# Optimization experiments

Hardware: AMD Instinct MI355X
Metric: run time of the kernel (lower is better)

Reference implementation:

```python
import jax, jax.numpy as jnp
import numpy as np

EPS = 1e-12  # torch F.normalize eps

def _conv1x1(x, w, b=None):
    # x: [B,C,H,W], w: [O,C] -> [B,O,H,W]
    y = jnp.einsum('bchw,oc->bohw', x, w)
    if b is not None:
        y = y + b[None, :, None, None]
    return y

def _l2norm(t):
    n = jnp.sqrt(jnp.sum(t * t, axis=-1, keepdims=True))
    return t / jnp.maximum(n, EPS)

def _gqa(x, w_qkv, w_proj, b_proj, heads=8):
    B, C, H, W = x.shape
    hd = C // heads
    S = H * W
    scale = hd ** -0.5
    qkv = _conv1x1(x, w_qkv)                       # [B,3C,H,W]
    qkv = qkv.reshape(B, 3, heads, hd, S)
    qkv = jnp.transpose(qkv, (0, 1, 2, 4, 3))      # [B,3,h,S,hd]
    q, k, v = qkv[:, 0], qkv[:, 1], qkv[:, 2]
    q = _l2norm(q)
    k = _l2norm(k)
    # group loop in original is just a partition of heads -> batch all heads
    attn = jnp.einsum('bhqd,bhkd->bhqk', q, k) * scale
    attn = jax.nn.softmax(attn, axis=-1)
    out = jnp.einsum('bhqk,bhkd->bhqd', attn, v)   # [B,h,S,hd]
    out = jnp.transpose(out, (0, 1, 3, 2)).reshape(B, C, H, W)
    return _conv1x1(out, w_proj, b_proj)

def _avg_pool(x, s):
    B, C, H, W = x.shape
    return x.reshape(B, C, H // s, s, W // s, s).mean(axis=(3, 5))

def _forward(x, w_qkv_l, w_proj_l, b_proj_l, w_qkv_g, w_proj_g, b_proj_g,
             w_f1, b_f1, w_f2, b_f2, stride=4, heads=8):
    local = _gqa(x, w_qkv_l, w_proj_l, b_proj_l, heads)
    xc = _avg_pool(x, stride)
    g = _gqa(xc, w_qkv_g, w_proj_g, b_proj_g, heads)
    B, C, H, W = x.shape
    g = jax.image.resize(g, (B, C, H, W), method='bilinear')  # half-pixel = align_corners=False
    h = _conv1x1(jnp.concatenate([local, g], axis=1), w_f1, b_f1)
    h = jax.nn.gelu(h, approximate=False)
    return _conv1x1(h, w_f2, b_f2)

def setup_inputs() -> dict:
    key = jax.random.key(0)
    ks = jax.random.split(key, 11)
    C = 256
    d = {
        'x': jax.random.normal(ks[0], (4, C, 48, 48), jnp.float32),
        'w_qkv_l': jax.random.normal(ks[1], (3 * C, C), jnp.float32) * 0.02,
        'w_proj_l': jax.random.normal(ks[2], (C, C), jnp.float32) * 0.02,
        'b_proj_l': jax.random.normal(ks[3], (C,), jnp.float32) * 0.02,
        'w_qkv_g': jax.random.normal(ks[4], (3 * C, C), jnp.float32) * 0.02,
        'w_proj_g': jax.random.normal(ks[5], (C, C), jnp.float32) * 0.02,
        'b_proj_g': jax.random.normal(ks[6], (C,), jnp.float32) * 0.02,
        'w_f1': jax.random.normal(ks[7], (C, 2 * C), jnp.float32) * 0.02,
        'b_f1': jax.random.normal(ks[8], (C,), jnp.float32) * 0.02,
        'w_f2': jax.random.normal(ks[9], (C, C), jnp.float32) * 0.02,
        'b_f2': jax.random.normal(ks[10], (C,), jnp.float32) * 0.02,
    }
    return d

def reference(x, w_qkv_l, w_proj_l, b_proj_l, w_qkv_g, w_proj_g, b_proj_g,
              w_f1, b_f1, w_f2, b_f2):
    return _forward(x, w_qkv_l, w_proj_l, b_proj_l, w_qkv_g, w_proj_g, b_proj_g,
                    w_f1, b_f1, w_f2, b_f2)
```

## Files before the change

kernel.cpp:

```cpp
#include <hip/hip_runtime.h>
#include <hip/hip_bf16.h>
#include <math.h>

typedef __attribute__((ext_vector_type(8))) short bf16x8;
typedef __attribute__((ext_vector_type(4))) float f32x4;

__device__ inline unsigned short f2bf(float x) {
  __hip_bfloat16 h = __float2bfloat16(x);
  return __builtin_bit_cast(unsigned short, h);
}
__device__ inline float bf2f(unsigned short u) {
  unsigned v = ((unsigned)u) << 16;
  return __builtin_bit_cast(float, v);
}
__device__ inline unsigned cvtpk(float a, float b) {
  unsigned r;
  asm("v_cvt_pk_bf16_f32 %0, %1, %2" : "=v"(r) : "v"(a), "v"(b));
  return r;
}

__global__ __launch_bounds__(256)
void prep_kernel(const float* __restrict__ w0, const float* __restrict__ w1,
                 const float* __restrict__ w2, const float* __restrict__ w3,
                 const float* __restrict__ w4, const float* __restrict__ w5,
                 unsigned short* __restrict__ d0, unsigned short* __restrict__ d1,
                 unsigned short* __restrict__ d2, unsigned short* __restrict__ d3,
                 unsigned short* __restrict__ d4, unsigned short* __restrict__ d5,
                 const float* __restrict__ x, float* __restrict__ xg) {
  int idx = blockIdx.x * 256 + threadIdx.x;
  if (idx < 22528) {
    int r = idx;
    const float* src; unsigned short* dst;
    if (r < 6144) { src = w0; dst = d0; }
    else if (r < 8192) { src = w1; dst = d1; r -= 6144; }
    else if (r < 14336) { src = w2; dst = d2; r -= 8192; }
    else if (r < 16384) { src = w3; dst = d3; r -= 14336; }
    else if (r < 20480) { src = w4; dst = d4; r -= 16384; }
    else { src = w5; dst = d5; r -= 20480; }
    const float* in = src + (size_t)r * 32;
    union { unsigned short u[32]; uint4 q[4]; } H, L;
#pragma unroll
    for (int i = 0; i < 32; ++i) {
      float v = in[i];
      unsigned short h = f2bf(v);
      H.u[i] = h;
      L.u[i] = f2bf(v - bf2f(h));
    }
    uint4* op = (uint4*)(dst + (size_t)r * 64);
#pragma unroll
    for (int q = 0; q < 4; ++q) { op[q] = H.q[q]; op[4 + q] = L.q[q]; }
  } else {
    int p = idx - 22528;
    if (p >= 4 * 256 * 144) return;
    int wc = p % 12;
    int t = p / 12;
    int hc = t % 12;
    int bc = t / 12;
    const float* src = x + ((size_t)bc * 48 + hc * 4) * 48 + wc * 4;
    float s = 0.f;
#pragma unroll
    for (int dy = 0; dy < 4; ++dy)
#pragma unroll
      for (int dx = 0; dx < 4; ++dx) s += src[dy * 48 + dx];
    xg[p] = s * (1.0f / 16.0f);
  }
}

template<int ACT, int OT, int CKS, int UPS, typename XT, typename YT>
__device__ __forceinline__
void conv_body(const unsigned short* __restrict__ Whl, const XT* __restrict__ X,
               const float* __restrict__ lpart, const float* __restrict__ bias,
               YT* __restrict__ Y, const float* __restrict__ gsm,
               int Cin, int S, size_t XbS, size_t YbS,
               int bx, int by, int bz, int tid) {
  constexpr int OI = OT / 64;
  __shared__ __align__(16) unsigned short Bs[64 * 32];
  const int w = tid >> 6, lane = tid & 63;
  const int g = lane >> 4, c = lane & 15;
  const int s0 = bx * 64;
  const int o0 = by * OT;
  const int b = bz;
  const int KB = Cin >> 5;
  const int sRow = tid & 63;
  const int jS = tid >> 6;
  const int ss = s0 + sRow;
  const bool sIn = (ss < S);
  unsigned short* BsRow = Bs + sRow * 32;
  const int hiOff = (jS ^ ((sRow >> 1) & 3)) * 8;

  int t00 = 0, t01 = 0, t10 = 0, t11 = 0;
  float w00 = 0.f, w01 = 0.f, w10 = 0.f, w11 = 0.f;
  if constexpr (UPS) {
    if (sIn) {
      int yo = ss / 48, xo = ss % 48;
      float sy = 0.25f * yo - 0.375f;
      float sx = 0.25f * xo - 0.375f;
      int y0 = (int)floorf(sy); float fy = sy - (float)y0;
      int x0 = (int)floorf(sx); float fx = sx - (float)x0;
      int y0c = min(11, max(0, y0)), y1c = min(11, max(0, y0 + 1));
      int x0c = min(11, max(0, x0)), x1c = min(11, max(0, x0 + 1));
      t00 = y0c * 12 + x0c; t01 = y0c * 12 + x1c;
      t10 = y1c * 12 + x0c; t11 = y1c * 12 + x1c;
      w00 = (1.f - fy) * (1.f - fx); w01 = (1.f - fy) * fx;
      w10 = fy * (1.f - fx);         w11 = fy * fx;
    }
  }

  f32x4 acc[OI][4];
#pragma unroll
  for (int oi = 0; oi < OI; ++oi)
#pragma unroll
    for (int si = 0; si < 4; ++si) acc[oi][si] = (f32x4){0.f, 0.f, 0.f, 0.f};

  for (int kb = 0; kb < KB; ++kb) {
    union { unsigned u[4]; bf16x8 v; } hu;
    if (sIn) {
      if constexpr (CKS > 0) {
        const float* xp = (const float*)X + (size_t)b * XbS +
                          (size_t)(kb * 32 + 8 * jS) * S + ss;
        const float* lp = lpart + ((size_t)b * 8 + kb) * S + ss;
        float den = 0.f;
        float num[8] = {0.f, 0.f, 0.f, 0.f, 0.f, 0.f, 0.f, 0.f};
#pragma unroll
        for (int ksi = 0; ksi < CKS; ++ksi) {
          den += lp[(size_t)ksi * 32 * S];
#pragma unroll
          for (int i = 0; i < 8; ++i)
            num[i] += xp[(size_t)(ksi * 1024 + i) * S];
        }
        float rd = 1.0f / den;
#pragma unroll
        for (int i = 0; i < 4; ++i)
          hu.u[i] = cvtpk(num[2 * i] * rd, num[2 * i + 1] * rd);
      } else if constexpr (UPS) {
        if (kb < 8) {
          const XT* xp = X + (size_t)b * XbS + (size_t)(kb * 32 + 8 * jS) * S + ss;
#pragma unroll
          for (int i = 0; i < 4; ++i) {
            unsigned lo = *(const unsigned short*)(xp + (size_t)(2 * i) * S);
            unsigned hi = *(const unsigned short*)(xp + (size_t)(2 * i + 1) * S);
            hu.u[i] = lo | (hi << 16);
          }
        } else {
          const float* gbb = gsm + (size_t)b * 256 * 144 +
                             (size_t)((kb - 8) * 32 + 8 * jS) * 144;
#pragma unroll
          for (int i = 0; i < 4; ++i) {
            const float* g0 = gbb + (size_t)(2 * i) * 144;
            const float* g1 = gbb + (size_t)(2 * i + 1) * 144;
            float v0 = w00 * g0[t00] + w01 * g0[t01] + w10 * g0[t10] + w11 * g0[t11];
            float v1 = w00 * g1[t00] + w01 * g1[t01] + w10 * g1[t10] + w11 * g1[t11];
            hu.u[i] = cvtpk(v0, v1);
          }
        }
      } else if constexpr (sizeof(XT) == 2) {
        const XT* xp = X + (size_t)b * XbS + (size_t)(kb * 32 + 8 * jS) * S + ss;
#pragma unroll
        for (int i = 0; i < 4; ++i) {
          unsigned lo = *(const unsigned short*)(xp + (size_t)(2 * i) * S);
          unsigned hi = *(const unsigned short*)(xp + (size_t)(2 * i + 1) * S);
          hu.u[i] = lo | (hi << 16);
        }
      } else {
        const float* xp = (const float*)X + (size_t)b * XbS +
                          (size_t)(kb * 32 + 8 * jS) * S + ss;
#pragma unroll
        for (int i = 0; i < 4; ++i)
          hu.u[i] = cvtpk(xp[(size_t)(2 * i) * S], xp[(size_t)(2 * i + 1) * S]);
      }
    } else {
#pragma unroll
      for (int i = 0; i < 4; ++i) hu.u[i] = 0;
    }
    bf16x8 ahi[OI], alo[OI];
#pragma unroll
    for (int oi = 0; oi < OI; ++oi) {
      const unsigned short* ap =
          Whl + ((size_t)(o0 + 16 * OI * w + 16 * oi + c) * KB + kb) * 64;
      ahi[oi] = *(const bf16x8*)(ap + 8 * g);
      alo[oi] = *(const bf16x8*)(ap + 32 + 8 * g);
    }
    __syncthreads();
    *(bf16x8*)(BsRow + hiOff) = hu.v;
    __syncthreads();
    bf16x8 bhi[4];
#pragma unroll
    for (int si = 0; si < 4; ++si) {
      int row = 16 * si + c;
      const unsigned short* bp = Bs + row * 32;
      bhi[si] = *(const bf16x8*)(bp + ((g ^ ((row >> 1) & 3)) * 8));
    }
#pragma unroll
    for (int oi = 0; oi < OI; ++oi)
#pragma unroll
      for (int si = 0; si < 4; ++si) {
        acc[oi][si] = __builtin_amdgcn_mfma_f32_16x16x32_bf16(ahi[oi], bhi[si], acc[oi][si], 0, 0, 0);
        acc[oi][si] = __builtin_amdgcn_mfma_f32_16x16x32_bf16(alo[oi], bhi[si], acc[oi][si], 0, 0, 0);
      }
  }
#pragma unroll
  for (int oi = 0; oi < OI; ++oi) {
#pragma unroll
    for (int r = 0; r < 4; ++r) {
      int o = o0 + 16 * OI * w + 16 * oi + 4 * g + r;
      float bv = bias ? bias[o] : 0.f;
#pragma unroll
      for (int si = 0; si < 4; ++si) {
        int s = s0 + 16 * si + c;
        if (s < S) {
          float v = acc[oi][si][r] + bv;
          if (ACT == 1) v = v * 0.5f * (1.0f + erff(v * 0.70710678118654752f));
          if constexpr (sizeof(YT) == 2)
            Y[(size_t)b * YbS + (size_t)o * S + s] = (YT)f2bf(v);
          else
            Y[(size_t)b * YbS + (size_t)o * S + s] = v;
        }
      }
    }
  }
}

__global__ __launch_bounds__(256)
void qkv_conv_kernel(const unsigned short* __restrict__ Wl, const float* __restrict__ Xl,
                     float* __restrict__ Yl,
                     const unsigned short* __restrict__ Wg, const float* __restrict__ Xg,
                     float* __restrict__ Yg) {
  if (blockIdx.y < 6) {
    conv_body<0, 128, 0, 0, float, float>(Wl, Xl, nullptr, nullptr, Yl, nullptr,
        256, 2304, (size_t)256 * 2304, (size_t)768 * 2304,
        blockIdx.x, blockIdx.y, blockIdx.z, threadIdx.x);
  } else {
    if (blockIdx.x >= 3) return;
    conv_body<0, 128, 0, 0, float, float>(Wg, Xg, nullptr, nullptr, Yg, nullptr,
        256, 144, (size_t)256 * 144, (size_t)768 * 144,
        blockIdx.x, blockIdx.y - 6, blockIdx.z, threadIdx.x);
  }
}

__global__ __launch_bounds__(256)
void proj_conv_kernel(const unsigned short* __restrict__ Wl, const float* __restrict__ opl,
                      const float* __restrict__ lpl, const float* __restrict__ bl,
                      unsigned short* __restrict__ cat,
                      const unsigned short* __restrict__ Wg, const float* __restrict__ opg,
                      const float* __restrict__ lpg, const float* __restrict__ bg,
                      float* __restrict__ gsm) {
  if (blockIdx.y < 4) {
    conv_body<0, 64, 3, 0, float, unsigned short>(Wl, opl, lpl, bl, cat, nullptr,
        256, 2304, (size_t)256 * 2304, (size_t)256 * 2304,
        blockIdx.x, blockIdx.y, blockIdx.z, threadIdx.x);
  } else {
    if (blockIdx.x >= 3) return;
    conv_body<0, 64, 3, 0, float, float>(Wg, opg, lpg, bg, gsm, nullptr,
        256, 144, (size_t)256 * 144, (size_t)256 * 144,
        blockIdx.x, blockIdx.y - 4, blockIdx.z, threadIdx.x);
  }
}

__global__ __launch_bounds__(256)
void f1_conv_kernel(const unsigned short* __restrict__ W, const unsigned short* __restrict__ cat,
                    const float* __restrict__ gsm, const float* __restrict__ bias,
                    unsigned short* __restrict__ hbuf) {
  conv_body<1, 64, 0, 1, unsigned short, unsigned short>(W, cat, nullptr, bias, hbuf, gsm,
      512, 2304, (size_t)256 * 2304, (size_t)256 * 2304,
      blockIdx.x, blockIdx.y, blockIdx.z, threadIdx.x);
}

__global__ __launch_bounds__(256)
void f2_conv_kernel(const unsigned short* __restrict__ W, const unsigned short* __restrict__ hbuf,
                    const float* __restrict__ bias, float* __restrict__ out) {
  conv_body<0, 64, 0, 0, unsigned short, float>(W, hbuf, nullptr, bias, out, nullptr,
      256, 2304, (size_t)256 * 2304, (size_t)256 * 2304,
      blockIdx.x, blockIdx.y, blockIdx.z, threadIdx.x);
}

__device__ __forceinline__
void l2n_body(const float* __restrict__ qkv, unsigned short* __restrict__ qd,
              unsigned short* __restrict__ kd, int S, int Sp, int idx) {
  int s = idx % Sp; int t = idx / Sp;
  int h = t & 7; t >>= 3;
  int qk = t & 1; int b = t >> 1;
  if (b >= 4) return;
  unsigned short* dst;
  int srow;
  if (qk == 0) { dst = qd; srow = s; }
  else {
    dst = kd;
    int blk = s >> 6, j = s & 63;
    srow = (blk << 6) + 32 * ((j >> 2) & 1) + 16 * (j >> 5) + 4 * ((j >> 3) & 3) + (j & 3);
  }
  unsigned wbuf[16];
  if (s < S) {
    const float* base = qkv + ((size_t)b * 768 + qk * 256 + h * 32) * S + s;
    float v[32]; float ss = 0.f;
#pragma unroll
    for (int d = 0; d < 32; ++d) { v[d] = base[(size_t)d * S]; ss += v[d] * v[d]; }
    float inv = 1.0f / fmaxf(sqrtf(ss), 1e-12f);
    if (qk == 0) inv *= 0.25506607138105343f;
#pragma unroll
    for (int i = 0; i < 16; ++i) wbuf[i] = cvtpk(v[2 * i] * inv, v[2 * i + 1] * inv);
  } else {
#pragma unroll
    for (int i = 0; i < 16; ++i) wbuf[i] = 0u;
  }
  uint4* o = (uint4*)(dst + ((size_t)(b * 8 + h) * Sp + srow) * 32);
#pragma unroll
  for (int i = 0; i < 4; ++i)
    o[i] = make_uint4(wbuf[4 * i], wbuf[4 * i + 1], wbuf[4 * i + 2], wbuf[4 * i + 3]);
}

__device__ __forceinline__
void vcvt_body(const float* __restrict__ qkv, unsigned short* __restrict__ vt,
               int S, int Sp, int idx) {
  int SpH = Sp >> 1;
  int sp = idx % SpH; int t = idx / SpH;
  int d = t & 31; t >>= 5;
  int h = t & 7; int b = t >> 3;
  if (b >= 4) return;
  const float* src = qkv + ((size_t)b * 768 + 512 + h * 32 + d) * S;
  int s2 = 2 * sp;
  float a = (s2 < S) ? src[s2] : 0.f;
  float c = (s2 + 1 < S) ? src[s2 + 1] : 0.f;
  *(unsigned*)(vt + ((size_t)(b * 8 + h) * 32 + d) * Sp + s2) = cvtpk(a, c);
}

__global__ __launch_bounds__(256)
void cvt_kernel(const float* __restrict__ qkv_l, unsigned short* __restrict__ qr_l,
                unsigned short* __restrict__ kr_l, unsigned short* __restrict__ vt_l,
                const float* __restrict__ qkv_g, unsigned short* __restrict__ qr_g,
                unsigned short* __restrict__ kr_g, unsigned short* __restrict__ vt_g) {
  const int L1 = 2 * 8 * 4 * 2304;
  const int L2 = 4 * 8 * 32 * 1152;
  const int L3 = 2 * 8 * 4 * 256;
  const int L4 = 4 * 8 * 32 * 128;
  int idx = blockIdx.x * 256 + threadIdx.x;
  if (idx < L1) l2n_body(qkv_l, qr_l, kr_l, 2304, 2304, idx);
  else if (idx < L1 + L2) vcvt_body(qkv_l, vt_l, 2304, 2304, idx - L1);
  else if (idx < L1 + L2 + L3) l2n_body(qkv_g, qr_g, kr_g, 144, 256, idx - L1 - L2);
  else if (idx < L1 + L2 + L3 + L4) vcvt_body(qkv_g, vt_g, 144, 256, idx - L1 - L2 - L3);
}

template<int KS>
__device__ __forceinline__
void attn_body(const unsigned short* __restrict__ qr, const unsigned short* __restrict__ kr,
               const unsigned short* __restrict__ vt, float* __restrict__ opart,
               float* __restrict__ lpart, int S, int Sp, int qblk, int ks,
               int h, int b, int tidx) {
  int w = tidx >> 6, lane = tidx & 63;
  int g = lane >> 4, c = lane & 15;
  int q0 = qblk * 256 + w * 64;
  const int chunks = Sp >> 6;
  const int c0 = (ks * chunks) / KS, c1 = ((ks + 1) * chunks) / KS;
  const unsigned short* qbh = qr + (size_t)(b * 8 + h) * Sp * 32;
  const unsigned short* kbh = kr + (size_t)(b * 8 + h) * Sp * 32;
  const unsigned short* vbh = vt + (size_t)(b * 8 + h) * 32 * Sp;

  bf16x8 qf[4];
#pragma unroll
  for (int f = 0; f < 4; ++f)
    qf[f] = *(const bf16x8*)(qbh + (size_t)(q0 + 16 * f + c) * 32 + 8 * g);

  f32x4 oacc[4][2];
#pragma unroll
  for (int f = 0; f < 4; ++f) {
    oacc[f][0] = (f32x4){0.f, 0.f, 0.f, 0.f};
    oacc[f][1] = (f32x4){0.f, 0.f, 0.f, 0.f};
  }
  float ls[4] = {0.f, 0.f, 0.f, 0.f};

  bf16x8 kf[4];
  {
    int k0 = c0 * 64;
#pragma unroll
    for (int t = 0; t < 4; ++t)
      kf[t] = *(const bf16x8*)(kbh + (size_t)(k0 + 16 * t + c) * 32 + 8 * g);
  }

  for (int ch = c0; ch < c1; ++ch) {
    int k0 = ch * 64;
    const f32x4 z = {0.f, 0.f, 0.f, 0.f};
    bool full = (k0 + 64 <= S);
    bf16x8 vf00 = *(const bf16x8*)(vbh + (size_t)c * Sp + k0 + 8 * g);
    bf16x8 vf01 = *(const bf16x8*)(vbh + (size_t)(16 + c) * Sp + k0 + 8 * g);
    bf16x8 vf10 = *(const bf16x8*)(vbh + (size_t)c * Sp + k0 + 32 + 8 * g);
    bf16x8 vf11 = *(const bf16x8*)(vbh + (size_t)(16 + c) * Sp + k0 + 32 + 8 * g);

    f32x4 sL[4], sH[4];
    __builtin_amdgcn_s_setprio(1);
#pragma unroll
    for (int f = 0; f < 4; ++f) {
      sL[f] = __builtin_amdgcn_mfma_f32_16x16x32_bf16(kf[0], qf[f], z, 0, 0, 0);
      sH[f] = __builtin_amdgcn_mfma_f32_16x16x32_bf16(kf[2], qf[f], z, 0, 0, 0);
    }
    __builtin_amdgcn_s_setprio(0);
    union { bf16x8 v; unsigned u[4]; } pf[4];
    if (full) {
#pragma unroll
      for (int f = 0; f < 4; ++f) {
        float e0 = __builtin_amdgcn_exp2f(sL[f][0]);
        float e1 = __builtin_amdgcn_exp2f(sL[f][1]);
        float e2 = __builtin_amdgcn_exp2f(sL[f][2]);
        float e3 = __builtin_amdgcn_exp2f(sL[f][3]);
        float e4 = __builtin_amdgcn_exp2f(sH[f][0]);
        float e5 = __builtin_amdgcn_exp2f(sH[f][1]);
        float e6 = __builtin_amdgcn_exp2f(sH[f][2]);
        float e7 = __builtin_amdgcn_exp2f(sH[f][3]);
        ls[f] += ((e0 + e1) + (e2 + e3)) + ((e4 + e5) + (e6 + e7));
        pf[f].u[0] = cvtpk(e0, e1); pf[f].u[1] = cvtpk(e2, e3);
        pf[f].u[2] = cvtpk(e4, e5); pf[f].u[3] = cvtpk(e6, e7);
      }
    } else {
#pragma unroll
      for (int f = 0; f < 4; ++f) {
        float e[8];
#pragma unroll
        for (int r = 0; r < 4; ++r) {
          int keyL = k0 + 8 * g + r;
          int keyH = k0 + 8 * g + 4 + r;
          e[r]     = (keyL < S) ? __builtin_amdgcn_exp2f(sL[f][r]) : 0.f;
          e[4 + r] = (keyH < S) ? __builtin_amdgcn_exp2f(sH[f][r]) : 0.f;
        }
        ls[f] += ((e[0] + e[1]) + (e[2] + e[3])) + ((e[4] + e[5]) + (e[6] + e[7]));
        pf[f].u[0] = cvtpk(e[0], e[1]); pf[f].u[1] = cvtpk(e[2], e[3]);
        pf[f].u[2] = cvtpk(e[4], e[5]); pf[f].u[3] = cvtpk(e[6], e[7]);
      }
    }
    __builtin_amdgcn_s_setprio(1);
#pragma unroll
    for (int f = 0; f < 4; ++f) {
      oacc[f][0] = __builtin_amdgcn_mfma_f32_16x16x32_bf16(vf00, pf[f].v, oacc[f][0], 0, 0, 0);
      oacc[f][1] = __builtin_amdgcn_mfma_f32_16x16x32_bf16(vf01, pf[f].v, oacc[f][1], 0, 0, 0);
    }
#pragma unroll
    for (int f = 0; f < 4; ++f) {
      sL[f] = __builtin_amdgcn_mfma_f32_16x16x32_bf16(kf[1], qf[f], z, 0, 0, 0);
      sH[f] = __builtin_amdgcn_mfma_f32_16x16x32_bf16(kf[3], qf[f], z, 0, 0, 0);
    }
    __builtin_amdgcn_s_setprio(0);
    if (ch + 1 < c1) {
      int kn = (ch + 1) * 64;
#pragma unroll
      for (int t = 0; t < 4; ++t)
        kf[t] = *(const bf16x8*)(kbh + (size_t)(kn + 16 * t + c) * 32 + 8 * g);
    }
    if (full) {
#pragma unroll
      for (int f = 0; f < 4; ++f) {
        float e0 = __builtin_amdgcn_exp2f(sL[f][0]);
        float e1 = __builtin_amdgcn_exp2f(sL[f][1]);
        float e2 = __builtin_amdgcn_exp2f(sL[f][2]);
        float e3 = __builtin_amdgcn_exp2f(sL[f][3]);
        float e4 = __builtin_amdgcn_exp2f(sH[f][0]);
        float e5 = __builtin_amdgcn_exp2f(sH[f][1]);
        float e6 = __builtin_amdgcn_exp2f(sH[f][2]);
        float e7 = __builtin_amdgcn_exp2f(sH[f][3]);
        ls[f] += ((e0 + e1) + (e2 + e3)) + ((e4 + e5) + (e6 + e7));
        pf[f].u[0] = cvtpk(e0, e1); pf[f].u[1] = cvtpk(e2, e3);
        pf[f].u[2] = cvtpk(e4, e5); pf[f].u[3] = cvtpk(e6, e7);
      }
    } else {
#pragma unroll
      for (int f = 0; f < 4; ++f) {
        float e[8];
#pragma unroll
        for (int r = 0; r < 4; ++r) {
          int keyL = k0 + 32 + 8 * g + r;
          int keyH = k0 + 32 + 8 * g + 4 + r;
          e[r]     = (keyL < S) ? __builtin_amdgcn_exp2f(sL[f][r]) : 0.f;
          e[4 + r] = (keyH < S) ? __builtin_amdgcn_exp2f(sH[f][r]) : 0.f;
        }
        ls[f] += ((e[0] + e[1]) + (e[2] + e[3])) + ((e[4] + e[5]) + (e[6] + e[7]));
        pf[f].u[0] = cvtpk(e[0], e[1]); pf[f].u[1] = cvtpk(e[2], e[3]);
        pf[f].u[2] = cvtpk(e[4], e[5]); pf[f].u[3] = cvtpk(e[6], e[7]);
      }
    }
    __builtin_amdgcn_s_setprio(1);
#pragma unroll
    for (int f = 0; f < 4; ++f) {
      oacc[f][0] = __builtin_amdgcn_mfma_f32_16x16x32_bf16(vf10, pf[f].v, oacc[f][0], 0, 0, 0);
      oacc[f][1] = __builtin_amdgcn_mfma_f32_16x16x32_bf16(vf11, pf[f].v, oacc[f][1], 0, 0, 0);
    }
    __builtin_amdgcn_s_setprio(0);
  }
#pragma unroll
  for (int f = 0; f < 4; ++f) {
    ls[f] += __shfl_xor(ls[f], 16, 64);
    ls[f] += __shfl_xor(ls[f], 32, 64);
  }
  size_t obase = ((size_t)(ks * 4 + b) * 256 + h * 32) * S;
#pragma unroll
  for (int f = 0; f < 4; ++f) {
    int q = q0 + 16 * f + c;
    if (q < S) {
#pragma unroll
      for (int r = 0; r < 4; ++r) {
        opart[obase + (size_t)(4 * g + r) * S + q]      = oacc[f][0][r];
        opart[obase + (size_t)(16 + 4 * g + r) * S + q] = oacc[f][1][r];
      }
    }
  }
  if (lane < 16) {
    size_t lb = ((size_t)(ks * 4 + b) * 8 + h) * S;
#pragma unroll
    for (int f = 0; f < 4; ++f)
      if (q0 + 16 * f + lane < S) lpart[lb + q0 + 16 * f + lane] = ls[f];
  }
}

__global__ __launch_bounds__(256)
void attn_merged_kernel(const unsigned short* __restrict__ qr_l,
                        const unsigned short* __restrict__ kr_l,
                        const unsigned short* __restrict__ vt_l,
                        float* __restrict__ op_l, float* __restrict__ lp_l,
                        const unsigned short* __restrict__ qr_g,
                        const unsigned short* __restrict__ kr_g,
                        const unsigned short* __restrict__ vt_g,
                        float* __restrict__ op_g, float* __restrict__ lp_g) {
  int h = blockIdx.x, b = blockIdx.z, y = blockIdx.y;
  if (y < 27)
    attn_body<3>(qr_l, kr_l, vt_l, op_l, lp_l, 2304, 2304, y / 3, y % 3, h, b, threadIdx.x);
  else
    attn_body<3>(qr_g, kr_g, vt_g, op_g, lp_g, 144, 256, 0, y - 27, h, b, threadIdx.x);
}

extern "C" void kernel_launch(void* const* d_in, const int* in_sizes, int n_in,
                              void* d_out, int out_size, void* d_ws, size_t ws_size,
                              hipStream_t stream) {
  const float* x        = (const float*)d_in[0];
  const float* w_qkv_l  = (const float*)d_in[1];
  const float* w_proj_l = (const float*)d_in[2];
  const float* b_proj_l = (const float*)d_in[3];
  const float* w_qkv_g  = (const float*)d_in[4];
  const float* w_proj_g = (const float*)d_in[5];
  const float* b_proj_g = (const float*)d_in[6];
  const float* w_f1     = (const float*)d_in[7];
  const float* b_f1     = (const float*)d_in[8];
  const float* w_f2     = (const float*)d_in[9];
  const float* b_f2     = (const float*)d_in[10];
  float* out = (float*)d_out;

  const int S = 2304, Sg = 144, B = 4;
  const int Sp = 2304, Sgp = 256;
  const int KS = 3;

  char* wsp = (char*)d_ws;
  size_t off = 0;
  auto alloc = [&](size_t bytes) { char* p = wsp + off; off = (off + bytes + 255) & ~(size_t)255; return p; };
  float* qkv_l = (float*)alloc((size_t)B * 768 * S * 4);
  unsigned short* cat = (unsigned short*)alloc((size_t)B * 256 * S * 2);
  unsigned short* hbuf = (unsigned short*)alloc((size_t)B * 256 * S * 2);
  float* xg    = (float*)alloc((size_t)B * 256 * Sg * 4);
  float* qkv_g = (float*)alloc((size_t)B * 768 * Sg * 4);
  float* gsm   = (float*)alloc((size_t)B * 256 * Sg * 4);
  unsigned short* qr_l = (unsigned short*)alloc((size_t)B * 8 * Sp * 32 * 2);
  unsigned short* kr_l = (unsigned short*)alloc((size_t)B * 8 * Sp * 32 * 2);
  unsigned short* vt_l = (unsigned short*)alloc((size_t)B * 8 * Sp * 32 * 2);
  unsigned short* qr_g = (unsigned short*)alloc((size_t)B * 8 * Sgp * 32 * 2);
  unsigned short* kr_g = (unsigned short*)alloc((size_t)B * 8 * Sgp * 32 * 2);
  unsigned short* vt_g = (unsigned short*)alloc((size_t)B * 8 * Sgp * 32 * 2);
  unsigned short* whl_qkv_l  = (unsigned short*)alloc((size_t)768 * 256 * 2 * 2);
  unsigned short* whl_proj_l = (unsigned short*)alloc((size_t)256 * 256 * 2 * 2);
  unsigned short* whl_qkv_g  = (unsigned short*)alloc((size_t)768 * 256 * 2 * 2);
  unsigned short* whl_proj_g = (unsigned short*)alloc((size_t)256 * 256 * 2 * 2);
  unsigned short* whl_f1     = (unsigned short*)alloc((size_t)256 * 512 * 2 * 2);
  unsigned short* whl_f2     = (unsigned short*)alloc((size_t)256 * 256 * 2 * 2);
  float* lpart_l = (float*)alloc((size_t)KS * B * 8 * S * 4);
  float* lpart_g = (float*)alloc((size_t)KS * B * 8 * Sg * 4);
  float* opart_l = qkv_l;
  float* opart_g = qkv_g;

  dim3 blk(256);

  prep_kernel<<<dim3(664), blk, 0, stream>>>(
      w_qkv_l, w_proj_l, w_qkv_g, w_proj_g, w_f1, w_f2,
      whl_qkv_l, whl_proj_l, whl_qkv_g, whl_proj_g, whl_f1, whl_f2, x, xg);

  qkv_conv_kernel<<<dim3(36, 12, B), blk, 0, stream>>>(
      whl_qkv_l, x, qkv_l, whl_qkv_g, xg, qkv_g);

  cvt_kernel<<<dim3(5760), blk, 0, stream>>>(
      qkv_l, qr_l, kr_l, vt_l, qkv_g, qr_g, kr_g, vt_g);

  attn_merged_kernel<<<dim3(8, 30, B), blk, 0, stream>>>(
      qr_l, kr_l, vt_l, opart_l, lpart_l, qr_g, kr_g, vt_g, opart_g, lpart_g);

  proj_conv_kernel<<<dim3(36, 8, B), blk, 0, stream>>>(
      whl_proj_l, opart_l, lpart_l, b_proj_l, cat,
      whl_proj_g, opart_g, lpart_g, b_proj_g, gsm);

  f1_conv_kernel<<<dim3(36, 4, B), blk, 0, stream>>>(
      whl_f1, cat, gsm, b_f1, hbuf);

  f2_conv_kernel<<<dim3(36, 4, B), blk, 0, stream>>>(
      whl_f2, hbuf, b_f2, out);
}
```

Measured before the change: 142.2 us.

## Fuse L2-normalize and bf16 conversion into QKV conv epilogue, drop cvt kernel

The QKV 1x1 conv now writes normalized, scaled bf16 Q and permuted K rows, plus transposed bf16 V, directly from its accumulators. This removes the separate cvt kernel and the fp32 qkv round trip through global memory. The attention kernel also computes the softmax row sums with an extra MFMA against a ones vector instead of scalar adds and shuffles, and gains a launch-bounds occupancy hint. In exchange, the conv epilogue does more per-block work and scattered 4-byte stores, and opart now needs its own workspace buffer.

Measured after the change: 210.5 us. 1.48x slower.

```diff
diff --git a/kernel.cpp b/kernel.cpp
--- a/kernel.cpp
+++ b/kernel.cpp
@@ -66,11 +66,13 @@
   }
 }
 
-template<int ACT, int OT, int CKS, int UPS, typename XT, typename YT>
+template<int ACT, int OT, int CKS, int UPS, int EPI, typename XT, typename YT>
 __device__ __forceinline__
 void conv_body(const unsigned short* __restrict__ Whl, const XT* __restrict__ X,
                const float* __restrict__ lpart, const float* __restrict__ bias,
                YT* __restrict__ Y, const float* __restrict__ gsm,
+               unsigned short* __restrict__ qd, unsigned short* __restrict__ kd,
+               unsigned short* __restrict__ vt, int Sp,
                int Cin, int S, size_t XbS, size_t YbS,
                int bx, int by, int bz, int tid) {
   constexpr int OI = OT / 64;
@@ -198,6 +200,60 @@
         acc[oi][si] = __builtin_amdgcn_mfma_f32_16x16x32_bf16(alo[oi], bhi[si], acc[oi][si], 0, 0, 0);
       }
   }
+
+  if constexpr (EPI == 1) {
+    int sec = o0 >> 8;
+    int h = ((o0 >> 5) & 7) + w;
+    if (sec == 2) {
+      unsigned short* vb = vt + (size_t)(b * 8 + h) * 32 * Sp;
+#pragma unroll
+      for (int oi = 0; oi < OI; ++oi)
+#pragma unroll
+        for (int r = 0; r < 4; ++r) {
+          int d = 16 * oi + 4 * g + r;
+#pragma unroll
+          for (int si = 0; si < 4; ++si) {
+            int s = s0 + 16 * si + c;
+            if (s < S) vb[(size_t)d * Sp + s] = f2bf(acc[oi][si][r]);
+          }
+        }
+    } else {
+      float invs[4];
+#pragma unroll
+      for (int si = 0; si < 4; ++si) {
+        float t = 0.f;
+#pragma unroll
+        for (int oi = 0; oi < OI; ++oi)
+#pragma unroll
+          for (int r = 0; r < 4; ++r) t += acc[oi][si][r] * acc[oi][si][r];
+        t += __shfl_xor(t, 16, 64);
+        t += __shfl_xor(t, 32, 64);
+        float inv = 1.0f / fmaxf(sqrtf(t), 1e-12f);
+        if (sec == 0) inv *= 0.25506607138105343f;
+        invs[si] = inv;
+      }
+      unsigned short* dstp = (sec == 0) ? qd : kd;
+#pragma unroll
+      for (int si = 0; si < 4; ++si) {
+        int s = s0 + 16 * si + c;
+        if (s >= S) continue;
+        int srow = s;
+        if (sec == 1) {
+          int blk2 = s >> 6, j = s & 63;
+          srow = (blk2 << 6) + 32 * ((j >> 2) & 1) + 16 * (j >> 5) + 4 * ((j >> 3) & 3) + (j & 3);
+        }
+        unsigned short* rowp = dstp + ((size_t)(b * 8 + h) * Sp + srow) * 32;
+#pragma unroll
+        for (int oi = 0; oi < OI; ++oi) {
+          int d0 = 16 * oi + 4 * g;
+          *(unsigned*)(rowp + d0)     = cvtpk(acc[oi][si][0] * invs[si], acc[oi][si][1] * invs[si]);
+          *(unsigned*)(rowp + d0 + 2) = cvtpk(acc[oi][si][2] * invs[si], acc[oi][si][3] * invs[si]);
+        }
+      }
+    }
+    return;
+  }
+
 #pragma unroll
   for (int oi = 0; oi < OI; ++oi) {
 #pragma unroll
@@ -222,17 +278,21 @@
 
 __global__ __launch_bounds__(256)
 void qkv_conv_kernel(const unsigned short* __restrict__ Wl, const float* __restrict__ Xl,
-                     float* __restrict__ Yl,
+                     unsigned short* __restrict__ qr_l, unsigned short* __restrict__ kr_l,
+                     unsigned short* __restrict__ vt_l,
                      const unsigned short* __restrict__ Wg, const float* __restrict__ Xg,
-                     float* __restrict__ Yg) {
+                     unsigned short* __restrict__ qr_g, unsigned short* __restrict__ kr_g,
+                     unsigned short* __restrict__ vt_g) {
   if (blockIdx.y < 6) {
-    conv_body<0, 128, 0, 0, float, float>(Wl, Xl, nullptr, nullptr, Yl, nullptr,
-        256, 2304, (size_t)256 * 2304, (size_t)768 * 2304,
+    conv_body<0, 128, 0, 0, 1, float, float>(Wl, Xl, nullptr, nullptr, (float*)nullptr, nullptr,
+        qr_l, kr_l, vt_l, 2304,
+        256, 2304, (size_t)256 * 2304, 0,
         blockIdx.x, blockIdx.y, blockIdx.z, threadIdx.x);
   } else {
     if (blockIdx.x >= 3) return;
-    conv_body<0, 128, 0, 0, float, float>(Wg, Xg, nullptr, nullptr, Yg, nullptr,
-        256, 144, (size_t)256 * 144, (size_t)768 * 144,
+    conv_body<0, 128, 0, 0, 1, float, float>(Wg, Xg, nullptr, nullptr, (float*)nullptr, nullptr,
+        qr_g, kr_g, vt_g, 256,
+        256, 144, (size_t)256 * 144, 0,
         blockIdx.x, blockIdx.y - 6, blockIdx.z, threadIdx.x);
   }
 }
@@ -245,12 +305,14 @@
                       const float* __restrict__ lpg, const float* __restrict__ bg,
                       float* __restrict__ gsm) {
   if (blockIdx.y < 4) {
-    conv_body<0, 64, 3, 0, float, unsigned short>(Wl, opl, lpl, bl, cat, nullptr,
+    conv_body<0, 64, 3, 0, 0, float, unsigned short>(Wl, opl, lpl, bl, cat, nullptr,
+        nullptr, nullptr, nullptr, 0,
         256, 2304, (size_t)256 * 2304, (size_t)256 * 2304,
         blockIdx.x, blockIdx.y, blockIdx.z, threadIdx.x);
   } else {
     if (blockIdx.x >= 3) return;
-    conv_body<0, 64, 3, 0, float, float>(Wg, opg, lpg, bg, gsm, nullptr,
+    conv_body<0, 64, 3, 0, 0, float, float>(Wg, opg, lpg, bg, gsm, nullptr,
+        nullptr, nullptr, nullptr, 0,
         256, 144, (size_t)256 * 144, (size_t)256 * 144,
         blockIdx.x, blockIdx.y - 4, blockIdx.z, threadIdx.x);
   }
@@ -260,7 +322,8 @@
 void f1_conv_kernel(const unsigned short* __restrict__ W, const unsigned short* __restrict__ cat,
                     const float* __restrict__ gsm, const float* __restrict__ bias,
                     unsigned short* __restrict__ hbuf) {
-  conv_body<1, 64, 0, 1, unsigned short, unsigned short>(W, cat, nullptr, bias, hbuf, gsm,
+  conv_body<1, 64, 0, 1, 0, unsigned short, unsigned short>(W, cat, nullptr, bias, hbuf, gsm,
+      nullptr, nullptr, nullptr, 0,
       512, 2304, (size_t)256 * 2304, (size_t)256 * 2304,
       blockIdx.x, blockIdx.y, blockIdx.z, threadIdx.x);
 }
@@ -268,75 +331,10 @@
 __global__ __launch_bounds__(256)
 void f2_conv_kernel(const unsigned short* __restrict__ W, const unsigned short* __restrict__ hbuf,
                     const float* __restrict__ bias, float* __restrict__ out) {
-  conv_body<0, 64, 0, 0, unsigned short, float>(W, hbuf, nullptr, bias, out, nullptr,
+  conv_body<0, 64, 0, 0, 0, unsigned short, float>(W, hbuf, nullptr, bias, out, nullptr,
+      nullptr, nullptr, nullptr, 0,
       256, 2304, (size_t)256 * 2304, (size_t)256 * 2304,
       blockIdx.x, blockIdx.y, blockIdx.z, threadIdx.x);
-}
-
-__device__ __forceinline__
-void l2n_body(const float* __restrict__ qkv, unsigned short* __restrict__ qd,
-              unsigned short* __restrict__ kd, int S, int Sp, int idx) {
-  int s = idx % Sp; int t = idx / Sp;
-  int h = t & 7; t >>= 3;
-  int qk = t & 1; int b = t >> 1;
-  if (b >= 4) return;
-  unsigned short* dst;
-  int srow;
-  if (qk == 0) { dst = qd; srow = s; }
-  else {
-    dst = kd;
-    int blk = s >> 6, j = s & 63;
-    srow = (blk << 6) + 32 * ((j >> 2) & 1) + 16 * (j >> 5) + 4 * ((j >> 3) & 3) + (j & 3);
-  }
-  unsigned wbuf[16];
-  if (s < S) {
-    const float* base = qkv + ((size_t)b * 768 + qk * 256 + h * 32) * S + s;
-    float v[32]; float ss = 0.f;
-#pragma unroll
-    for (int d = 0; d < 32; ++d) { v[d] = base[(size_t)d * S]; ss += v[d] * v[d]; }
-    float inv = 1.0f / fmaxf(sqrtf(ss), 1e-12f);
-    if (qk == 0) inv *= 0.25506607138105343f;
-#pragma unroll
-    for (int i = 0; i < 16; ++i) wbuf[i] = cvtpk(v[2 * i] * inv, v[2 * i + 1] * inv);
-  } else {
-#pragma unroll
-    for (int i = 0; i < 16; ++i) wbuf[i] = 0u;
-  }
-  uint4* o = (uint4*)(dst + ((size_t)(b * 8 + h) * Sp + srow) * 32);
-#pragma unroll
-  for (int i = 0; i < 4; ++i)
-    o[i] = make_uint4(wbuf[4 * i], wbuf[4 * i + 1], wbuf[4 * i + 2], wbuf[4 * i + 3]);
-}
-
-__device__ __forceinline__
-void vcvt_body(const float* __restrict__ qkv, unsigned short* __restrict__ vt,
-               int S, int Sp, int idx) {
-  int SpH = Sp >> 1;
-  int sp = idx % SpH; int t = idx / SpH;
-  int d = t & 31; t >>= 5;
-  int h = t & 7; int b = t >> 3;
-  if (b >= 4) return;
-  const float* src = qkv + ((size_t)b * 768 + 512 + h * 32 + d) * S;
-  int s2 = 2 * sp;
-  float a = (s2 < S) ? src[s2] : 0.f;
-  float c = (s2 + 1 < S) ? src[s2 + 1] : 0.f;
-  *(unsigned*)(vt + ((size_t)(b * 8 + h) * 32 + d) * Sp + s2) = cvtpk(a, c);
-}
-
-__global__ __launch_bounds__(256)
-void cvt_kernel(const float* __restrict__ qkv_l, unsigned short* __restrict__ qr_l,
-                unsigned short* __restrict__ kr_l, unsigned short* __restrict__ vt_l,
-                const float* __restrict__ qkv_g, unsigned short* __restrict__ qr_g,
-                unsigned short* __restrict__ kr_g, unsigned short* __restrict__ vt_g) {
-  const int L1 = 2 * 8 * 4 * 2304;
-  const int L2 = 4 * 8 * 32 * 1152;
-  const int L3 = 2 * 8 * 4 * 256;
-  const int L4 = 4 * 8 * 32 * 128;
-  int idx = blockIdx.x * 256 + threadIdx.x;
-  if (idx < L1) l2n_body(qkv_l, qr_l, kr_l, 2304, 2304, idx);
-  else if (idx < L1 + L2) vcvt_body(qkv_l, vt_l, 2304, 2304, idx - L1);
-  else if (idx < L1 + L2 + L3) l2n_body(qkv_g, qr_g, kr_g, 144, 256, idx - L1 - L2);
-  else if (idx < L1 + L2 + L3 + L4) vcvt_body(qkv_g, vt_g, 144, 256, idx - L1 - L2 - L3);
 }
 
 template<int KS>
@@ -359,13 +357,17 @@
   for (int f = 0; f < 4; ++f)
     qf[f] = *(const bf16x8*)(qbh + (size_t)(q0 + 16 * f + c) * 32 + 8 * g);
 
-  f32x4 oacc[4][2];
+  union { unsigned u[4]; bf16x8 v; } onesu;
+#pragma unroll
+  for (int i = 0; i < 4; ++i) onesu.u[i] = 0x3F803F80u;
+
+  f32x4 oacc[4][2], lacc[4];
 #pragma unroll
   for (int f = 0; f < 4; ++f) {
     oacc[f][0] = (f32x4){0.f, 0.f, 0.f, 0.f};
     oacc[f][1] = (f32x4){0.f, 0.f, 0.f, 0.f};
-  }
-  float ls[4] = {0.f, 0.f, 0.f, 0.f};
+    lacc[f]    = (f32x4){0.f, 0.f, 0.f, 0.f};
+  }
 
   bf16x8 kf[4];
   {
@@ -404,7 +406,6 @@
         float e5 = __builtin_amdgcn_exp2f(sH[f][1]);
         float e6 = __builtin_amdgcn_exp2f(sH[f][2]);
         float e7 = __builtin_amdgcn_exp2f(sH[f][3]);
-        ls[f] += ((e0 + e1) + (e2 + e3)) + ((e4 + e5) + (e6 + e7));
         pf[f].u[0] = cvtpk(e0, e1); pf[f].u[1] = cvtpk(e2, e3);
         pf[f].u[2] = cvtpk(e4, e5); pf[f].u[3] = cvtpk(e6, e7);
       }
@@ -419,7 +420,6 @@
           e[r]     = (keyL < S) ? __builtin_amdgcn_exp2f(sL[f][r]) : 0.f;
           e[4 + r] = (keyH < S) ? __builtin_amdgcn_exp2f(sH[f][r]) : 0.f;
         }
-        ls[f] += ((e[0] + e[1]) + (e[2] + e[3])) + ((e[4] + e[5]) + (e[6] + e[7]));
         pf[f].u[0] = cvtpk(e[0], e[1]); pf[f].u[1] = cvtpk(e[2], e[3]);
         pf[f].u[2] = cvtpk(e[4], e[5]); pf[f].u[3] = cvtpk(e[6], e[7]);
       }
@@ -429,6 +429,7 @@
     for (int f = 0; f < 4; ++f) {
       oacc[f][0] = __builtin_amdgcn_mfma_f32_16x16x32_bf16(vf00, pf[f].v, oacc[f][0], 0, 0, 0);
       oacc[f][1] = __builtin_amdgcn_mfma_f32_16x16x32_bf16(vf01, pf[f].v, oacc[f][1], 0, 0, 0);
+      lacc[f]    = __builtin_amdgcn_mfma_f32_16x16x32_bf16(onesu.v, pf[f].v, lacc[f], 0, 0, 0);
     }
 #pragma unroll
     for (int f = 0; f < 4; ++f) {
@@ -453,7 +454,6 @@
         float e5 = __builtin_amdgcn_exp2f(sH[f][1]);
         float e6 = __builtin_amdgcn_exp2f(sH[f][2]);
         float e7 = __builtin_amdgcn_exp2f(sH[f][3]);
-        ls[f] += ((e0 + e1) + (e2 + e3)) + ((e4 + e5) + (e6 + e7));
         pf[f].u[0] = cvtpk(e0, e1); pf[f].u[1] = cvtpk(e2, e3);
         pf[f].u[2] = cvtpk(e4, e5); pf[f].u[3] = cvtpk(e6, e7);
       }
@@ -468,7 +468,6 @@
           e[r]     = (keyL < S) ? __builtin_amdgcn_exp2f(sL[f][r]) : 0.f;
           e[4 + r] = (keyH < S) ? __builtin_amdgcn_exp2f(sH[f][r]) : 0.f;
         }
-        ls[f] += ((e[0] + e[1]) + (e[2] + e[3])) + ((e[4] + e[5]) + (e[6] + e[7]));
         pf[f].u[0] = cvtpk(e[0], e[1]); pf[f].u[1] = cvtpk(e[2], e[3]);
         pf[f].u[2] = cvtpk(e[4], e[5]); pf[f].u[3] = cvtpk(e[6], e[7]);
       }
@@ -478,13 +477,9 @@
     for (int f = 0; f < 4; ++f) {
       oacc[f][0] = __builtin_amdgcn_mfma_f32_16x16x32_bf16(vf10, pf[f].v, oacc[f][0], 0, 0, 0);
       oacc[f][1] = __builtin_amdgcn_mfma_f32_16x16x32_bf16(vf11, pf[f].v, oacc[f][1], 0, 0, 0);
+      lacc[f]    = __builtin_amdgcn_mfma_f32_16x16x32_bf16(onesu.v, pf[f].v, lacc[f], 0, 0, 0);
     }
     __builtin_amdgcn_s_setprio(0);
-  }
-#pragma unroll
-  for (int f = 0; f < 4; ++f) {
-    ls[f] += __shfl_xor(ls[f], 16, 64);
-    ls[f] += __shfl_xor(ls[f], 32, 64);
   }
   size_t obase = ((size_t)(ks * 4 + b) * 256 + h * 32) * S;
 #pragma unroll
@@ -502,11 +497,11 @@
     size_t lb = ((size_t)(ks * 4 + b) * 8 + h) * S;
 #pragma unroll
     for (int f = 0; f < 4; ++f)
-      if (q0 + 16 * f + lane < S) lpart[lb + q0 + 16 * f + lane] = ls[f];
-  }
-}
-
-__global__ __launch_bounds__(256)
+      if (q0 + 16 * f + lane < S) lpart[lb + q0 + 16 * f + lane] = lacc[f][0];
+  }
+}
+
+__global__ __launch_bounds__(256, 4)
 void attn_merged_kernel(const unsigned short* __restrict__ qr_l,
                         const unsigned short* __restrict__ kr_l,
                         const unsigned short* __restrict__ vt_l,
@@ -545,11 +540,11 @@
   char* wsp = (char*)d_ws;
   size_t off = 0;
   auto alloc = [&](size_t bytes) { char* p = wsp + off; off = (off + bytes + 255) & ~(size_t)255; return p; };
-  float* qkv_l = (float*)alloc((size_t)B * 768 * S * 4);
+  float* opart_l = (float*)alloc((size_t)KS * B * 256 * S * 4);
   unsigned short* cat = (unsigned short*)alloc((size_t)B * 256 * S * 2);
   unsigned short* hbuf = (unsigned short*)alloc((size_t)B * 256 * S * 2);
   float* xg    = (float*)alloc((size_t)B * 256 * Sg * 4);
-  float* qkv_g = (float*)alloc((size_t)B * 768 * Sg * 4);
+  float* opart_g = (float*)alloc((size_t)KS * B * 256 * Sg * 4);
   float* gsm   = (float*)alloc((size_t)B * 256 * Sg * 4);
   unsigned short* qr_l = (unsigned short*)alloc((size_t)B * 8 * Sp * 32 * 2);
   unsigned short* kr_l = (unsigned short*)alloc((size_t)B * 8 * Sp * 32 * 2);
@@ -565,8 +560,6 @@
   unsigned short* whl_f2     = (unsigned short*)alloc((size_t)256 * 256 * 2 * 2);
   float* lpart_l = (float*)alloc((size_t)KS * B * 8 * S * 4);
   float* lpart_g = (float*)alloc((size_t)KS * B * 8 * Sg * 4);
-  float* opart_l = qkv_l;
-  float* opart_g = qkv_g;
 
   dim3 blk(256);
 
@@ -575,10 +568,8 @@
       whl_qkv_l, whl_proj_l, whl_qkv_g, whl_proj_g, whl_f1, whl_f2, x, xg);
 
   qkv_conv_kernel<<<dim3(36, 12, B), blk, 0, stream>>>(
-      whl_qkv_l, x, qkv_l, whl_qkv_g, xg, qkv_g);
-
-  cvt_kernel<<<dim3(5760), blk, 0, stream>>>(
-      qkv_l, qr_l, kr_l, vt_l, qkv_g, qr_g, kr_g, vt_g);
+      whl_qkv_l, x, qr_l, kr_l, vt_l,
+      whl_qkv_g, xg, qr_g, kr_g, vt_g);
 
   attn_merged_kernel<<<dim3(8, 30, B), blk, 0, stream>>>(
       qr_l, kr_l, vt_l, opart_l, lpart_l, qr_g, kr_g, vt_g, opart_g, lpart_g);
```
